# Kernel optimization log

Measured on AMD Instinct MI355X. Metric: run time of the kernel, lower is better.

The kernel has to match this reference:

```python
import jax, jax.numpy as jnp
import numpy as np

N_NODES = 100000
N_EDGES = 1600000
EMD_DIM = 64
EPS = 1e-12  # F.normalize eps


def setup_inputs() -> dict:
    key = jax.random.key(0)
    ks = jax.random.split(key, 7)
    x = jax.random.normal(ks[0], (N_NODES, EMD_DIM), dtype=jnp.float32)
    W = jax.random.normal(ks[1], (EMD_DIM, EMD_DIM), dtype=jnp.float32) * (1.0 / np.sqrt(EMD_DIM))
    b = jax.random.normal(ks[2], (EMD_DIM,), dtype=jnp.float32) * 0.02
    wc = jax.random.normal(ks[3], (EMD_DIM,), dtype=jnp.float32) * (1.0 / np.sqrt(EMD_DIM))
    bc = jax.random.normal(ks[4], (1,), dtype=jnp.float32) * 0.02
    src = jax.random.randint(ks[5], (N_EDGES,), 0, N_NODES, dtype=jnp.int32)
    dst = jax.random.randint(ks[6], (N_EDGES,), 0, N_NODES, dtype=jnp.int32)
    return {"x": x, "W": W, "b": b, "wc": wc, "bc": bc, "src": src, "dst": dst}


def reference(x, W, b, wc, bc, src, dst):
    # gnn2: DGL GraphConv(norm='none', activation=None):
    #   y = sum_{(u->v) in E} (x @ W)[u]  scattered into v, plus bias.
    y = x @ W                                   # [N, D] dense transform first (D small)
    msg = y[src]                                # [E, D] gather
    agg = jax.ops.segment_sum(msg, dst, num_segments=x.shape[0])  # [N, D] scatter-add
    h = agg + b
    # F.normalize(h, p=2, dim=1)
    norm = jnp.linalg.norm(h, axis=1, keepdims=True)
    h = h / jnp.maximum(norm, EPS)
    # dgl.mean_nodes -> mean over all nodes; classifier Linear(D, 1).squeeze(-1)
    graph_repr = jnp.mean(h, axis=0)            # [D]
    logits = graph_repr @ wc + bc[0]            # scalar
    # emb dict is just contiguous slices of h (h2dict); h carries all embeddings.
    return logits, h
```

## Files before the change

kernel.cpp:

```cpp
#include <hip/hip_runtime.h>

#define NN 100000
#define NE 1600000
#define D 64
#define NB ((NN + 255) / 256)
#define SCAN2_T 512

__global__ __launch_bounds__(256) void degree_hist(const int* __restrict__ dst,
                                                   int* __restrict__ deg) {
    const int n4 = NE / 4;
    for (int i = blockIdx.x * blockDim.x + threadIdx.x; i < n4;
         i += gridDim.x * blockDim.x) {
        const int4 d = reinterpret_cast<const int4*>(dst)[i];
        atomicAdd(&deg[d.x], 1);
        atomicAdd(&deg[d.y], 1);
        atomicAdd(&deg[d.z], 1);
        atomicAdd(&deg[d.w], 1);
    }
}

__global__ __launch_bounds__(256) void scan1(const int* __restrict__ deg,
                                             int* __restrict__ partial,
                                             int* __restrict__ blockSums) {
    const int t = threadIdx.x;
    const int i = blockIdx.x * 256 + t;
    const int lane = t & 63, wid = t >> 6;
    const int orig = (i < NN) ? deg[i] : 0;
    int v = orig;
#pragma unroll
    for (int off = 1; off < 64; off <<= 1) {
        int n = __shfl_up(v, off, 64);
        if (lane >= off) v += n;
    }
    __shared__ int wsum[4];
    if (lane == 63) wsum[wid] = v;
    __syncthreads();
    if (t == 0) {
        int s = 0;
#pragma unroll
        for (int w = 0; w < 4; ++w) { int tmp = wsum[w]; wsum[w] = s; s += tmp; }
    }
    __syncthreads();
    const int incl = v + wsum[wid];
    if (i < NN) partial[i] = incl - orig;
    if (t == 255) blockSums[blockIdx.x] = incl;
}

__global__ __launch_bounds__(SCAN2_T) void scan2(int* __restrict__ blockSums) {
    __shared__ int sm[SCAN2_T];
    const int t = threadIdx.x;
    const int orig = (t < NB) ? blockSums[t] : 0;
    sm[t] = orig;
    __syncthreads();
    for (int off = 1; off < SCAN2_T; off <<= 1) {
        int v = (t >= off) ? sm[t - off] : 0;
        __syncthreads();
        sm[t] += v;
        __syncthreads();
    }
    if (t < NB) blockSums[t] = sm[t] - orig;
}

__global__ __launch_bounds__(256) void scan3(const int* __restrict__ partial,
                                             const int* __restrict__ blockSums,
                                             int* __restrict__ offs,
                                             int* __restrict__ cursor) {
    const int i = blockIdx.x * 256 + threadIdx.x;
    if (i < NN) {
        const int o = partial[i] + blockSums[blockIdx.x];
        offs[i] = o;
        cursor[i] = o;
    }
}

__global__ __launch_bounds__(256) void bucket_fill(const int* __restrict__ src,
                                                   const int* __restrict__ dst,
                                                   int* __restrict__ cursor,
                                                   int* __restrict__ csr) {
    const int n4 = NE / 4;
    for (int i = blockIdx.x * blockDim.x + threadIdx.x; i < n4;
         i += gridDim.x * blockDim.x) {
        const int4 d = reinterpret_cast<const int4*>(dst)[i];
        const int4 s = reinterpret_cast<const int4*>(src)[i];
        csr[atomicAdd(&cursor[d.x], 1)] = s.x;
        csr[atomicAdd(&cursor[d.y], 1)] = s.y;
        csr[atomicAdd(&cursor[d.z], 1)] = s.z;
        csr[atomicAdd(&cursor[d.w], 1)] = s.w;
    }
}

__global__ __launch_bounds__(256) void gather_transform_norm(
        const float* __restrict__ x, const int* __restrict__ csr,
        const int* __restrict__ offs, const int* __restrict__ deg,
        const float* __restrict__ W, const float* __restrict__ b,
        float* __restrict__ h, float* __restrict__ colsum) {
    const int lane = threadIdx.x & 63;
    const int wid  = threadIdx.x >> 6;
    const int grp  = lane >> 4;
    const int sub  = lane & 15;

    __shared__ float Wt[64 * 65];
    __shared__ float smem[4][64];
    for (int idx = threadIdx.x; idx < 64 * 64; idx += 256) {
        const int k = idx >> 6, l = idx & 63;
        Wt[l * 65 + k] = W[idx];
    }
    __syncthreads();
    const float bj = b[lane];
    const float* wrow = &Wt[lane * 65];

    const int waveId = (blockIdx.x * blockDim.x + threadIdx.x) >> 6;
    const int nWaves = (gridDim.x * blockDim.x) >> 6;
    float csum = 0.f;
    for (int node = waveId; node < NN; node += nWaves) {
        const int start = offs[node];
        const int cnt   = deg[node];
        float ax = 0.f, ay = 0.f, az = 0.f, aw = 0.f;
        for (int c0 = 0; c0 < cnt; c0 += 64) {
            const int pos  = start + c0 + lane;
            const int idxv = (pos < NE) ? csr[pos] : 0;
            const int m = (cnt - c0 < 64) ? (cnt - c0) : 64;
#pragma unroll 4
            for (int j = 0; j < m; j += 4) {
                const int e = j + grp;
                const int s = __shfl(idxv, e, 64);
                if (e < m) {
                    const float4 v = *reinterpret_cast<const float4*>(
                        x + (size_t)s * D + 4 * sub);
                    ax += v.x; ay += v.y; az += v.z; aw += v.w;
                }
            }
        }
#pragma unroll
        for (int off = 16; off <= 32; off <<= 1) {
            ax += __shfl_xor(ax, off, 64);
            ay += __shfl_xor(ay, off, 64);
            az += __shfl_xor(az, off, 64);
            aw += __shfl_xor(aw, off, 64);
        }
        float v = bj;
#pragma unroll
        for (int k0 = 0; k0 < 16; ++k0) {
            const float a0 = __shfl(ax, k0, 64);
            const float a1 = __shfl(ay, k0, 64);
            const float a2 = __shfl(az, k0, 64);
            const float a3 = __shfl(aw, k0, 64);
            v = fmaf(a0, wrow[4 * k0 + 0], v);
            v = fmaf(a1, wrow[4 * k0 + 1], v);
            v = fmaf(a2, wrow[4 * k0 + 2], v);
            v = fmaf(a3, wrow[4 * k0 + 3], v);
        }
        float ss = v * v;
#pragma unroll
        for (int off = 32; off > 0; off >>= 1) ss += __shfl_xor(ss, off, 64);
        v = v / fmaxf(sqrtf(ss), 1e-12f);
        h[(size_t)node * D + lane] = v;
        csum += v;
    }
    smem[wid][lane] = csum;
    __syncthreads();
    if (wid == 0) {
        const float t = smem[0][lane] + smem[1][lane] + smem[2][lane] + smem[3][lane];
        atomicAdd(&colsum[lane], t);
    }
}

__global__ void finalize(const float* __restrict__ colsum,
                         const float* __restrict__ wc,
                         const float* __restrict__ bc,
                         float* __restrict__ out0) {
    const int lane = threadIdx.x;
    float v = colsum[lane] * (1.0f / (float)NN) * wc[lane];
#pragma unroll
    for (int off = 32; off > 0; off >>= 1) v += __shfl_xor(v, off, 64);
    if (lane == 0) out0[0] = v + bc[0];
}

extern "C" void kernel_launch(void* const* d_in, const int* in_sizes, int n_in,
                              void* d_out, int out_size, void* d_ws, size_t ws_size,
                              hipStream_t stream) {
    const float* x   = (const float*)d_in[0];
    const float* W   = (const float*)d_in[1];
    const float* b   = (const float*)d_in[2];
    const float* wc  = (const float*)d_in[3];
    const float* bc  = (const float*)d_in[4];
    const int*   src = (const int*)d_in[5];
    const int*   dst = (const int*)d_in[6];

    float* out = (float*)d_out;
    float* h   = out + 1;

    int*   deg       = (int*)d_ws;
    int*   partial   = deg + NN;
    int*   offs      = partial + NN;
    int*   cursor    = offs + NN;
    int*   blockSums = cursor + NN;
    float* colsum    = (float*)(blockSums + SCAN2_T);
    int*   csr       = (int*)(colsum + 64);

    hipMemsetAsync(deg, 0, NN * sizeof(int), stream);
    hipMemsetAsync(colsum, 0, 64 * sizeof(float), stream);

    degree_hist<<<2048, 256, 0, stream>>>(dst, deg);
    scan1<<<NB, 256, 0, stream>>>(deg, partial, blockSums);
    scan2<<<1, SCAN2_T, 0, stream>>>(blockSums);
    scan3<<<NB, 256, 0, stream>>>(partial, blockSums, offs, cursor);
    bucket_fill<<<2048, 256, 0, stream>>>(src, dst, cursor, csr);
    gather_transform_norm<<<2048, 256, 0, stream>>>(x, csr, offs, deg, W, b, h, colsum);
    finalize<<<1, 64, 0, stream>>>(colsum, wc, bc, out);
}
```

Measured before the change: 428.0 us.

## Split degree and cursor counters into 8 sub-histograms to spread atomics

Degree counting and CSR bucket fill now use 8 separate counter arrays, picked by edge-chunk index, so atomics on the same node spread across different addresses. The scan now runs over the interleaved (node, sub) array so each node's sub-buckets stay contiguous, and it produces a node offset array with a sentinel so degree comes from adjacent offsets. The gather kernel grid is also doubled. The cost is an 8x larger memset and scan, which adds memory traffic that has to be paid back by less atomic contention.

```diff
diff --git a/kernel.cpp b/kernel.cpp
--- a/kernel.cpp
+++ b/kernel.cpp
@@ -3,95 +3,106 @@
 #define NN 100000
 #define NE 1600000
 #define D 64
-#define NB ((NN + 255) / 256)
-#define SCAN2_T 512
+#define NK 8
+#define M (NN * NK)
+#define SCAN_BS 1024
+#define NBA ((M + SCAN_BS - 1) / SCAN_BS)
 
 __global__ __launch_bounds__(256) void degree_hist(const int* __restrict__ dst,
-                                                   int* __restrict__ deg) {
+                                                   int* __restrict__ deg8) {
     const int n4 = NE / 4;
     for (int i = blockIdx.x * blockDim.x + threadIdx.x; i < n4;
          i += gridDim.x * blockDim.x) {
         const int4 d = reinterpret_cast<const int4*>(dst)[i];
-        atomicAdd(&deg[d.x], 1);
-        atomicAdd(&deg[d.y], 1);
-        atomicAdd(&deg[d.z], 1);
-        atomicAdd(&deg[d.w], 1);
-    }
-}
-
-__global__ __launch_bounds__(256) void scan1(const int* __restrict__ deg,
-                                             int* __restrict__ partial,
-                                             int* __restrict__ blockSums) {
+        int* dk = deg8 + (size_t)(i & 7) * NN;
+        atomicAdd(&dk[d.x], 1);
+        atomicAdd(&dk[d.y], 1);
+        atomicAdd(&dk[d.z], 1);
+        atomicAdd(&dk[d.w], 1);
+    }
+}
+
+__global__ __launch_bounds__(SCAN_BS) void scanA(const int* __restrict__ deg8,
+                                                 int* __restrict__ cursor8,
+                                                 int* __restrict__ bsum) {
     const int t = threadIdx.x;
-    const int i = blockIdx.x * 256 + t;
+    const int i = blockIdx.x * SCAN_BS + t;
     const int lane = t & 63, wid = t >> 6;
-    const int orig = (i < NN) ? deg[i] : 0;
-    int v = orig;
+    int orig = 0, slot = 0;
+    if (i < M) {
+        const int v = i >> 3, k = i & 7;
+        slot = k * NN + v;
+        orig = deg8[slot];
+    }
+    int val = orig;
 #pragma unroll
     for (int off = 1; off < 64; off <<= 1) {
-        int n = __shfl_up(v, off, 64);
-        if (lane >= off) v += n;
-    }
-    __shared__ int wsum[4];
-    if (lane == 63) wsum[wid] = v;
+        int n = __shfl_up(val, off, 64);
+        if (lane >= off) val += n;
+    }
+    __shared__ int wsum[16];
+    if (lane == 63) wsum[wid] = val;
     __syncthreads();
     if (t == 0) {
         int s = 0;
 #pragma unroll
-        for (int w = 0; w < 4; ++w) { int tmp = wsum[w]; wsum[w] = s; s += tmp; }
-    }
-    __syncthreads();
-    const int incl = v + wsum[wid];
-    if (i < NN) partial[i] = incl - orig;
-    if (t == 255) blockSums[blockIdx.x] = incl;
-}
-
-__global__ __launch_bounds__(SCAN2_T) void scan2(int* __restrict__ blockSums) {
-    __shared__ int sm[SCAN2_T];
+        for (int w = 0; w < 16; ++w) { int tmp = wsum[w]; wsum[w] = s; s += tmp; }
+    }
+    __syncthreads();
+    const int incl = val + wsum[wid];
+    if (i < M) cursor8[slot] = incl - orig;
+    if (t == SCAN_BS - 1) bsum[blockIdx.x] = incl;
+}
+
+__global__ __launch_bounds__(SCAN_BS) void scanB(int* __restrict__ bsum) {
+    __shared__ int sm[SCAN_BS];
     const int t = threadIdx.x;
-    const int orig = (t < NB) ? blockSums[t] : 0;
+    const int orig = (t < NBA) ? bsum[t] : 0;
     sm[t] = orig;
     __syncthreads();
-    for (int off = 1; off < SCAN2_T; off <<= 1) {
+    for (int off = 1; off < SCAN_BS; off <<= 1) {
         int v = (t >= off) ? sm[t - off] : 0;
         __syncthreads();
         sm[t] += v;
         __syncthreads();
     }
-    if (t < NB) blockSums[t] = sm[t] - orig;
-}
-
-__global__ __launch_bounds__(256) void scan3(const int* __restrict__ partial,
-                                             const int* __restrict__ blockSums,
-                                             int* __restrict__ offs,
-                                             int* __restrict__ cursor) {
-    const int i = blockIdx.x * 256 + threadIdx.x;
-    if (i < NN) {
-        const int o = partial[i] + blockSums[blockIdx.x];
-        offs[i] = o;
-        cursor[i] = o;
-    }
+    if (t < NBA) bsum[t] = sm[t] - orig;
+}
+
+__global__ __launch_bounds__(SCAN_BS) void scanC(int* __restrict__ cursor8,
+                                                 const int* __restrict__ bsum,
+                                                 int* __restrict__ offs_node) {
+    const int i = blockIdx.x * SCAN_BS + threadIdx.x;
+    if (i < M) {
+        const int v = i >> 3, k = i & 7;
+        const int slot = k * NN + v;
+        const int o = cursor8[slot] + bsum[blockIdx.x];
+        cursor8[slot] = o;
+        if (k == 0) offs_node[v] = o;
+    }
+    if (i == 0) offs_node[NN] = NE;
 }
 
 __global__ __launch_bounds__(256) void bucket_fill(const int* __restrict__ src,
                                                    const int* __restrict__ dst,
-                                                   int* __restrict__ cursor,
+                                                   int* __restrict__ cursor8,
                                                    int* __restrict__ csr) {
     const int n4 = NE / 4;
     for (int i = blockIdx.x * blockDim.x + threadIdx.x; i < n4;
          i += gridDim.x * blockDim.x) {
         const int4 d = reinterpret_cast<const int4*>(dst)[i];
         const int4 s = reinterpret_cast<const int4*>(src)[i];
-        csr[atomicAdd(&cursor[d.x], 1)] = s.x;
-        csr[atomicAdd(&cursor[d.y], 1)] = s.y;
-        csr[atomicAdd(&cursor[d.z], 1)] = s.z;
-        csr[atomicAdd(&cursor[d.w], 1)] = s.w;
+        int* cur = cursor8 + (size_t)(i & 7) * NN;
+        csr[atomicAdd(&cur[d.x], 1)] = s.x;
+        csr[atomicAdd(&cur[d.y], 1)] = s.y;
+        csr[atomicAdd(&cur[d.z], 1)] = s.z;
+        csr[atomicAdd(&cur[d.w], 1)] = s.w;
     }
 }
 
 __global__ __launch_bounds__(256) void gather_transform_norm(
         const float* __restrict__ x, const int* __restrict__ csr,
-        const int* __restrict__ offs, const int* __restrict__ deg,
+        const int* __restrict__ offs_node,
         const float* __restrict__ W, const float* __restrict__ b,
         float* __restrict__ h, float* __restrict__ colsum) {
     const int lane = threadIdx.x & 63;
@@ -113,8 +124,8 @@
     const int nWaves = (gridDim.x * blockDim.x) >> 6;
     float csum = 0.f;
     for (int node = waveId; node < NN; node += nWaves) {
-        const int start = offs[node];
-        const int cnt   = deg[node];
+        const int start = offs_node[node];
+        const int cnt   = offs_node[node + 1] - start;
         float ax = 0.f, ay = 0.f, az = 0.f, aw = 0.f;
         for (int c0 = 0; c0 < cnt; c0 += 64) {
             const int pos  = start + c0 + lane;
@@ -190,22 +201,21 @@
     float* out = (float*)d_out;
     float* h   = out + 1;
 
-    int*   deg       = (int*)d_ws;
-    int*   partial   = deg + NN;
-    int*   offs      = partial + NN;
-    int*   cursor    = offs + NN;
-    int*   blockSums = cursor + NN;
-    float* colsum    = (float*)(blockSums + SCAN2_T);
+    int*   deg8      = (int*)d_ws;
+    int*   cursor8   = deg8 + M;
+    int*   bsum      = cursor8 + M;
+    int*   offs_node = bsum + SCAN_BS;
+    float* colsum    = (float*)(offs_node + NN + 1);
     int*   csr       = (int*)(colsum + 64);
 
-    hipMemsetAsync(deg, 0, NN * sizeof(int), stream);
+    hipMemsetAsync(deg8, 0, (size_t)M * sizeof(int), stream);
     hipMemsetAsync(colsum, 0, 64 * sizeof(float), stream);
 
-    degree_hist<<<2048, 256, 0, stream>>>(dst, deg);
-    scan1<<<NB, 256, 0, stream>>>(deg, partial, blockSums);
-    scan2<<<1, SCAN2_T, 0, stream>>>(blockSums);
-    scan3<<<NB, 256, 0, stream>>>(partial, blockSums, offs, cursor);
-    bucket_fill<<<2048, 256, 0, stream>>>(src, dst, cursor, csr);
-    gather_transform_norm<<<2048, 256, 0, stream>>>(x, csr, offs, deg, W, b, h, colsum);
+    degree_hist<<<2048, 256, 0, stream>>>(dst, deg8);
+    scanA<<<NBA, SCAN_BS, 0, stream>>>(deg8, cursor8, bsum);
+    scanB<<<1, SCAN_BS, 0, stream>>>(bsum);
+    scanC<<<NBA, SCAN_BS, 0, stream>>>(cursor8, bsum, offs_node);
+    bucket_fill<<<2048, 256, 0, stream>>>(src, dst, cursor8, csr);
+    gather_transform_norm<<<4096, 256, 0, stream>>>(x, csr, offs_node, W, b, h, colsum);
     finalize<<<1, 64, 0, stream>>>(colsum, wc, bc, out);
 }
```

Measured after the change: 427.6 us. About the same (-0.1%).
